# Kernel optimization log

Measured on AMD Instinct MI355X. Metric: run time of the kernel, lower is better.

Reference implementation:

```python
import jax, jax.numpy as jnp
import numpy as np

N_NODES = 50000
N_FEAT = 128
HID = 128
OUT = 64


def setup_inputs() -> dict:
    key = jax.random.key(0)
    ks = jax.random.split(key, 16)
    T, N, F, H, O, E = 8, N_NODES, N_FEAT, HID, OUT, 600000
    s = lambda fan: 1.0 / np.sqrt(fan)
    inp = {
        "x_sequence": jax.random.normal(ks[0], (T, N, F), dtype=jnp.float32),
        "edge_index_sequence": jax.random.randint(ks[1], (T, 2, E), 0, N, dtype=jnp.int64),
        # GCN layer 1 and 2 (weight + bias, PyG GCNConv style)
        "W1": jax.random.uniform(ks[2], (F, H), jnp.float32, -s(F), s(F)),
        "b1": jnp.zeros((H,), jnp.float32),
        "W2": jax.random.uniform(ks[3], (H, H), jnp.float32, -s(H), s(H)),
        "b2": jnp.zeros((H,), jnp.float32),
        # LSTM (single layer, gate order i,f,g,o like torch)
        "Wih": jax.random.uniform(ks[4], (4 * H, H), jnp.float32, -s(H), s(H)),
        "Whh": jax.random.uniform(ks[5], (4 * H, H), jnp.float32, -s(H), s(H)),
        "bih": jax.random.uniform(ks[6], (4 * H,), jnp.float32, -s(H), s(H)),
        "bhh": jax.random.uniform(ks[7], (4 * H,), jnp.float32, -s(H), s(H)),
        # output head
        "Wout": jax.random.uniform(ks[8], (H, O), jnp.float32, -s(H), s(H)),
        "bout": jnp.zeros((O,), jnp.float32),
    }
    return inp


def _gcn(x, src, dst, W, b, n_nodes):
    # GCNConv: add self-loops, symmetric normalization D^-1/2 A D^-1/2
    self_idx = jnp.arange(n_nodes)
    s = jnp.concatenate([src, self_idx])
    d = jnp.concatenate([dst, self_idx])
    deg = jax.ops.segment_sum(jnp.ones(s.shape, x.dtype), d, num_segments=n_nodes)
    dinv = jnp.where(deg > 0, jax.lax.rsqrt(deg), 0.0)
    xw = x @ W                                  # [N,H] transform before aggregation
    coef = (dinv[s] * dinv[d])[:, None]         # [E+N,1]
    agg = jax.ops.segment_sum(xw[s] * coef, d, num_segments=n_nodes)
    return agg + b


def reference(x_sequence, edge_index_sequence, W1, b1, W2, b2,
              Wih, Whh, bih, bhh, Wout, bout):
    T, N, F = x_sequence.shape
    H = Whh.shape[1]

    # spatial GCN stack per timestep (dropout is identity at inference)
    def spatial(carry, inp):
        x_t, ei = inp
        src, dst = ei[0], ei[1]
        h = jax.nn.relu(_gcn(x_t, src, dst, W1, b1, N))
        h = jax.nn.relu(_gcn(h, src, dst, W2, b2, N))
        return carry, h

    _, emb = jax.lax.scan(spatial, None, (x_sequence, edge_index_sequence))  # [T,N,H]

    # LSTM over time, batch = N nodes
    def lstm_step(carry, x_t):
        h, c = carry
        g = x_t @ Wih.T + h @ Whh.T + bih + bhh
        i, f, gg, o = jnp.split(g, 4, axis=-1)
        c = jax.nn.sigmoid(f) * c + jax.nn.sigmoid(i) * jnp.tanh(gg)
        h = jax.nn.sigmoid(o) * jnp.tanh(c)
        return (h, c), None

    h0 = jnp.zeros((N, H), x_sequence.dtype)
    c0 = jnp.zeros((N, H), x_sequence.dtype)
    (hT, cT), _ = jax.lax.scan(lstm_step, (h0, c0), emb)

    final = hT                      # lstm_out[:, -1, :] == last hidden state
    output = final @ Wout + bout    # [N, output_dim]
    return output, hT, cT
```

## Files before the change

kernel.cpp:

```cpp
#include <hip/hip_runtime.h>
#include <math.h>

#define TSTEPS 8
#define FDIM 128
#define HDIM 128
#define ODIM 64
#define GDIM 512
#define BUCKR 2048
#define BUCKR_SHIFT 11
#define BPT 32

typedef __attribute__((ext_vector_type(4))) float f32x4;
typedef __attribute__((ext_vector_type(8))) short s8;

__device__ __forceinline__ float sigmf(float x) { return 1.0f / (1.0f + __expf(-x)); }
__device__ __forceinline__ float fast_tanh(float x) {
    float ax = fabsf(x);
    float ez = __expf(2.f * ax);
    float r = 1.f - 2.f / (ez + 1.f);
    return copysignf(r, x);
}

__device__ __forceinline__ ushort f2bf(float x) {
    uint u = __float_as_uint(x);
    u += 0x7FFFu + ((u >> 16) & 1u);
    return (ushort)(u >> 16);
}
__device__ __forceinline__ float bf2f(ushort h) { return __uint_as_float(((uint)h) << 16); }


__global__ void prep_lstm_w(const float* __restrict__ wih, const float* __restrict__ whh,
                            const float* __restrict__ bih, const float* __restrict__ bhh,
                            float* __restrict__ wcat, float* __restrict__ bsum) {
    int idx = blockIdx.x * 256 + threadIdx.x;
    if (idx < 256 * GDIM) {
        int k = idx >> 9;
        int col = idx & 511;
        float v = (k < HDIM) ? wih[col * HDIM + k] : whh[col * HDIM + (k - HDIM)];
        wcat[idx] = v;
        if (k == 0) bsum[col] = bih[col] + bhh[col];
    }
}

__global__ void pack_b(const float* __restrict__ B, int K, int NC,
                       uint* __restrict__ hi, uint* __restrict__ lo) {
    int total = (K / 32) * (NC / 16) * 256;
    int idx = blockIdx.x * 256 + threadIdx.x;
    if (idx >= total) return;
    int d = idx & 3, l = (idx >> 2) & 63, t = idx >> 8;
    int NT = NC / 16;
    int kt = t / NT, nt = t % NT;
    int k = kt * 32 + (l >> 4) * 8 + d * 2;
    int col = nt * 16 + (l & 15);
    float va = B[(size_t)k * NC + col];
    float vb = B[(size_t)(k + 1) * NC + col];
    ushort ha = f2bf(va), hb = f2bf(vb);
    float ra = va - bf2f(ha), rb = vb - bf2f(hb);
    hi[idx] = (uint)ha | ((uint)hb << 16);
    lo[idx] = (uint)f2bf(ra) | ((uint)f2bf(rb) << 16);
}

__global__ void zero_int(int* __restrict__ p, int n) {
    int idx = blockIdx.x * 256 + threadIdx.x;
    if (idx < n) p[idx] = 0;
}


__global__ __launch_bounds__(256) void bin_count(const int* __restrict__ edges,
                                                 int* __restrict__ gcount,
                                                 int E, int N, int nbuck) {
    __shared__ int h[1024];
    int tid = threadIdx.x;
    int t = blockIdx.x >> 5, b = blockIdx.x & 31;
    int ce = (E + BPT - 1) / BPT;
    int e0 = b * ce, e1 = min(e0 + ce, E);
    for (int i = tid; i < 1024; i += 256) h[i] = 0;
    __syncthreads();
    const int* dstp = edges + (size_t)t * 2 * E + E;
    for (int i = e0 + tid; i < e1; i += 256) {
        int gid = t * N + dstp[i];
        atomicAdd(&h[gid >> BUCKR_SHIFT], 1);
    }
    __syncthreads();
    for (int i = tid; i < nbuck; i += 256) {
        int c = h[i];
        if (c) atomicAdd(&gcount[i], c);
    }
}

__global__ __launch_bounds__(1024) void scan_buckets(const int* __restrict__ gcount,
                                                     int* __restrict__ bucket_start,
                                                     int* __restrict__ bucket_cursor,
                                                     int nbuck, int* __restrict__ row_start,
                                                     int nTotal, int totalE) {
    __shared__ int s[1024];
    int t = threadIdx.x;
    int own = (t < nbuck) ? gcount[t] : 0;
    s[t] = own; __syncthreads();
    for (int off = 1; off < 1024; off <<= 1) {
        int add = (t >= off) ? s[t - off] : 0;
        __syncthreads();
        s[t] += add;
        __syncthreads();
    }
    if (t < nbuck) {
        int excl = s[t] - own;
        bucket_start[t] = excl;
        bucket_cursor[t] = excl;
    }
    if (t == 0) {
        bucket_start[nbuck] = totalE;
        row_start[nTotal] = totalE;
    }
}

__global__ __launch_bounds__(256) void bin_scatter(const int* __restrict__ edges,
                                                   int* __restrict__ bucket_cursor,
                                                   uint2* __restrict__ staged,
                                                   int E, int N, int nbuck) {
    __shared__ int h[1024];
    __shared__ int base[1024];
    int tid = threadIdx.x;
    int t = blockIdx.x >> 5, b = blockIdx.x & 31;
    int ce = (E + BPT - 1) / BPT;
    int e0 = b * ce, e1 = min(e0 + ce, E);
    for (int i = tid; i < 1024; i += 256) h[i] = 0;
    __syncthreads();
    const int* srcp = edges + (size_t)t * 2 * E;
    const int* dstp = srcp + E;
    for (int i = e0 + tid; i < e1; i += 256) {
        int gid = t * N + dstp[i];
        atomicAdd(&h[gid >> BUCKR_SHIFT], 1);
    }
    __syncthreads();
    for (int i = tid; i < nbuck; i += 256) {
        int c = h[i];
        if (c) base[i] = atomicAdd(&bucket_cursor[i], c);
        h[i] = 0;
    }
    __syncthreads();
    for (int i = e0 + tid; i < e1; i += 256) {
        int sgid = t * N + srcp[i];
        int dgid = t * N + dstp[i];
        int bk = dgid >> BUCKR_SHIFT;
        int loc = atomicAdd(&h[bk], 1);
        staged[base[bk] + loc] = make_uint2((uint)sgid, (uint)dgid);
    }
}

__global__ __launch_bounds__(256) void bin_csr(const uint2* __restrict__ staged,
                                               const int* __restrict__ bucket_start,
                                               int* __restrict__ row_start,
                                               int* __restrict__ csr_src,
                                               float* __restrict__ dinv, int nTotal) {
    __shared__ int cnt[BUCKR];
    __shared__ int part[256];
    int tid = threadIdx.x;
    int node0 = blockIdx.x << BUCKR_SHIFT;
    int nloc = min(BUCKR, nTotal - node0);
    int ebase = bucket_start[blockIdx.x], eend = bucket_start[blockIdx.x + 1];

    for (int j = tid; j < BUCKR; j += 256) cnt[j] = 0;
    __syncthreads();
    for (int e = ebase + tid; e < eend; e += 256)
        atomicAdd(&cnt[(int)staged[e].y - node0], 1);
    __syncthreads();

    int s = 0;
    #pragma unroll
    for (int k = 0; k < 8; k++) s += cnt[tid * 8 + k];
    part[tid] = s; __syncthreads();
    for (int off = 1; off < 256; off <<= 1) {
        int add = (tid >= off) ? part[tid - off] : 0;
        __syncthreads();
        part[tid] += add;
        __syncthreads();
    }
    int run = part[tid] - s;
    #pragma unroll
    for (int k = 0; k < 8; k++) {
        int j = tid * 8 + k;
        int c = cnt[j];
        if (j < nloc) {
            row_start[node0 + j] = ebase + run;
            dinv[node0 + j] = rsqrtf((float)(c + 1));
        }
        cnt[j] = run;
        run += c;
    }
    __syncthreads();
    for (int e = ebase + tid; e < eend; e += 256) {
        uint2 ed = staged[e];
        int d = (int)ed.y - node0;
        int pos = ebase + atomicAdd(&cnt[d], 1);
        csr_src[pos] = (int)ed.x;
    }
}


__global__ __launch_bounds__(256) void agg_gather_t(
    const int* __restrict__ row_start, const int* __restrict__ csr_src,
    const uint* __restrict__ xh, const uint* __restrict__ xl,
    const float* __restrict__ dinv, const float* __restrict__ bias,
    uint* __restrict__ ohi, uint* __restrict__ olo, int rowOff, int nloc)
{
    int w = (blockIdx.x * 256 + threadIdx.x) >> 6;
    int lane = threadIdx.x & 63;
    if (w >= nloc) return;
    int wg = rowOff + w;
    float dr = dinv[wg];
    float cc = dr * dr;
    uint shv = xh[(size_t)wg * 64 + lane];
    uint slv = xl[(size_t)wg * 64 + lane];
    float a0 = (__uint_as_float(shv << 16) + __uint_as_float(slv << 16)) * cc;
    float a1 = (__uint_as_float(shv & 0xFFFF0000u) + __uint_as_float(slv & 0xFFFF0000u)) * cc;
    int e = row_start[wg], e1 = row_start[wg + 1];
    for (; e + 4 <= e1; e += 4) {
        int s0 = csr_src[e], s1 = csr_src[e + 1], s2 = csr_src[e + 2], s3 = csr_src[e + 3];
        float c0 = dinv[s0] * dr, c1 = dinv[s1] * dr, c2 = dinv[s2] * dr, c3 = dinv[s3] * dr;
        uint u0 = xh[(size_t)s0 * 64 + lane];
        uint u1 = xh[(size_t)s1 * 64 + lane];
        uint u2 = xh[(size_t)s2 * 64 + lane];
        uint u3 = xh[(size_t)s3 * 64 + lane];
        a0 = fmaf(__uint_as_float(u0 << 16), c0, a0);
        a1 = fmaf(__uint_as_float(u0 & 0xFFFF0000u), c0, a1);
        a0 = fmaf(__uint_as_float(u1 << 16), c1, a0);
        a1 = fmaf(__uint_as_float(u1 & 0xFFFF0000u), c1, a1);
        a0 = fmaf(__uint_as_float(u2 << 16), c2, a0);
        a1 = fmaf(__uint_as_float(u2 & 0xFFFF0000u), c2, a1);
        a0 = fmaf(__uint_as_float(u3 << 16), c3, a0);
        a1 = fmaf(__uint_as_float(u3 & 0xFFFF0000u), c3, a1);
    }
    for (; e < e1; e++) {
        int s = csr_src[e];
        float cf = dinv[s] * dr;
        uint u = xh[(size_t)s * 64 + lane];
        a0 = fmaf(__uint_as_float(u << 16), cf, a0);
        a1 = fmaf(__uint_as_float(u & 0xFFFF0000u), cf, a1);
    }
    float2 b = ((const float2*)bias)[lane];
    a0 = fmaxf(a0 + b.x, 0.f);
    a1 = fmaxf(a1 + b.y, 0.f);
    ushort h0 = f2bf(a0), h1 = f2bf(a1);
    ohi[(size_t)wg * 64 + lane] = (uint)h0 | ((uint)h1 << 16);
    olo[(size_t)wg * 64 + lane] = (uint)f2bf(a0 - bf2f(h0)) | ((uint)f2bf(a1 - bf2f(h1)) << 16);
}


template<bool SPLITSRC>
__global__ __launch_bounds__(512) void gemm_mfma128(
    const float* __restrict__ A32, const ushort* __restrict__ Ahi, const ushort* __restrict__ Alo,
    const uint4* __restrict__ Bhi, const uint4* __restrict__ Blo,
    ushort* __restrict__ Chi, ushort* __restrict__ Clo, int nrows)
{
    __shared__ ushort AsH[128][136];
    __shared__ ushort AsL[128][136];
    const int r0 = blockIdx.x * 128;
    const int tid = threadIdx.x;

    if (SPLITSRC) {
        for (int v = tid; v < 128 * 16; v += 512) {
            int row = v >> 4, seg = v & 15;
            uint4 h = make_uint4(0, 0, 0, 0), L = make_uint4(0, 0, 0, 0);
            if (r0 + row < nrows) {
                h = *(const uint4*)(Ahi + (size_t)(r0 + row) * 128 + seg * 8);
                L = *(const uint4*)(Alo + (size_t)(r0 + row) * 128 + seg * 8);
            }
            *(uint4*)&AsH[row][seg * 8] = h;
            *(uint4*)&AsL[row][seg * 8] = L;
        }
    } else {
        for (int v = tid; v < 128 * 16; v += 512) {
            int row = v >> 4, seg = v & 15;
            float4 a = make_float4(0.f, 0.f, 0.f, 0.f), b = a;
            if (r0 + row < nrows) {
                const float4* src = (const float4*)A32 + (size_t)(r0 + row) * 32 + seg * 2;
                a = src[0]; b = src[1];
            }
            float vv[8] = {a.x, a.y, a.z, a.w, b.x, b.y, b.z, b.w};
            uint hh[4], ll[4];
            #pragma unroll
            for (int i = 0; i < 4; i++) {
                float v0 = vv[2 * i], v1 = vv[2 * i + 1];
                ushort h0 = f2bf(v0), h1 = f2bf(v1);
                hh[i] = (uint)h0 | ((uint)h1 << 16);
                ll[i] = (uint)f2bf(v0 - bf2f(h0)) | ((uint)f2bf(v1 - bf2f(h1)) << 16);
            }
            *(uint4*)&AsH[row][seg * 8] = make_uint4(hh[0], hh[1], hh[2], hh[3]);
            *(uint4*)&AsL[row][seg * 8] = make_uint4(ll[0], ll[1], ll[2], ll[3]);
        }
    }
    __syncthreads();

    const int l = tid & 63, w = tid >> 6;
    const int wm = w & 3, wn = w >> 2;
    const int lrow = l & 15, lk = (l >> 4) * 8;

    f32x4 acc[2][4];
    #pragma unroll
    for (int m = 0; m < 2; m++)
        #pragma unroll
        for (int p = 0; p < 4; p++) acc[m][p] = (f32x4){0.f, 0.f, 0.f, 0.f};

    #pragma unroll
    for (int kt = 0; kt < 4; kt++) {
        uint4 BH[4], BL[4];
        #pragma unroll
        for (int p = 0; p < 4; p++) {
            int nt = 4 * wn + p;
            BH[p] = Bhi[(kt * 8 + nt) * 64 + l];
            BL[p] = Blo[(kt * 8 + nt) * 64 + l];
        }
        s8 aH[2], aL[2];
        #pragma unroll
        for (int m = 0; m < 2; m++) {
            int row = (2 * wm + m) * 16 + lrow;
            aH[m] = *(const s8*)&AsH[row][kt * 32 + lk];
            aL[m] = *(const s8*)&AsL[row][kt * 32 + lk];
        }
        #pragma unroll
        for (int p = 0; p < 4; p++) {
            s8 bh = __builtin_bit_cast(s8, BH[p]);
            s8 bl = __builtin_bit_cast(s8, BL[p]);
            #pragma unroll
            for (int m = 0; m < 2; m++) {
                acc[m][p] = __builtin_amdgcn_mfma_f32_16x16x32_bf16(aH[m], bh, acc[m][p], 0, 0, 0);
                acc[m][p] = __builtin_amdgcn_mfma_f32_16x16x32_bf16(aH[m], bl, acc[m][p], 0, 0, 0);
                acc[m][p] = __builtin_amdgcn_mfma_f32_16x16x32_bf16(aL[m], bh, acc[m][p], 0, 0, 0);
            }
        }
    }

    __syncthreads();
    const int lr4 = (l >> 4) * 4;
    #pragma unroll
    for (int m = 0; m < 2; m++) {
        #pragma unroll
        for (int p = 0; p < 4; p++) {
            int col = (4 * wn + p) * 16 + lrow;
            #pragma unroll
            for (int r = 0; r < 4; r++) {
                int row = (2 * wm + m) * 16 + lr4 + r;
                float v = acc[m][p][r];
                ushort h = f2bf(v);
                AsH[row][col] = h;
                AsL[row][col] = f2bf(v - bf2f(h));
            }
        }
    }
    __syncthreads();
    for (int v = tid; v < 128 * 16; v += 512) {
        int row = v >> 4, seg = v & 15;
        if (r0 + row < nrows) {
            *(uint4*)(Chi + (size_t)(r0 + row) * 128 + seg * 8) = *(const uint4*)&AsH[row][seg * 8];
            *(uint4*)(Clo + (size_t)(r0 + row) * 128 + seg * 8) = *(const uint4*)&AsL[row][seg * 8];
        }
    }
}


template<bool LAST>
__global__ __launch_bounds__(512, 4) void lstm_step_t(
    const ushort* __restrict__ Ehi, const ushort* __restrict__ Elo,
    ushort* __restrict__ Hhi, ushort* __restrict__ Hlo,
    const uint4* __restrict__ Bhi, const uint4* __restrict__ Blo,
    const float* __restrict__ bsum, float* __restrict__ cbuf,
    const uint4* __restrict__ Whi, const uint4* __restrict__ Wlo,
    const float* __restrict__ bout,
    float* __restrict__ outp, float* __restrict__ outh, float* __restrict__ outc,
    int nrows)
{
    __shared__ ushort AsH[32][264];
    __shared__ ushort AsL[32][264];
    const int r0 = blockIdx.x * 32;
    const int tid = threadIdx.x;
    const int l = tid & 63, w = tid >> 6;
    const int lrow = l & 15, lk = (l >> 4) * 8, lr4 = (l >> 4) * 4;

    for (int v = tid; v < 32 * 32; v += 512) {
        int row = v >> 5, seg = v & 31;
        uint4 h = make_uint4(0, 0, 0, 0), L = make_uint4(0, 0, 0, 0);
        if (r0 + row < nrows) {
            if (seg < 16) {
                size_t g = (size_t)(r0 + row) * 128 + seg * 8;
                h = *(const uint4*)(Ehi + g);
                L = *(const uint4*)(Elo + g);
            } else {
                size_t g = (size_t)(r0 + row) * 128 + (seg - 16) * 8;
                h = *(const uint4*)(Hhi + g);
                L = *(const uint4*)(Hlo + g);
            }
        }
        *(uint4*)&AsH[row][seg * 8] = h;
        *(uint4*)&AsL[row][seg * 8] = L;
    }
    __syncthreads();

    f32x4 acc[2][4];
    #pragma unroll
    for (int m = 0; m < 2; m++)
        #pragma unroll
        for (int q = 0; q < 4; q++) {
            float b = bsum[q * 128 + 16 * w + lrow];
            acc[m][q] = (f32x4){b, b, b, b};
        }

    #pragma unroll 2
    for (int kt = 0; kt < 8; kt++) {
        uint4 BH[4], BL[4];
        #pragma unroll
        for (int q = 0; q < 4; q++) {
            int nt = 8 * q + w;
            BH[q] = Bhi[((size_t)kt * 32 + nt) * 64 + l];
            BL[q] = Blo[((size_t)kt * 32 + nt) * 64 + l];
        }
        s8 aH[2], aL[2];
        #pragma unroll
        for (int m = 0; m < 2; m++) {
            int row = m * 16 + lrow;
            aH[m] = *(const s8*)&AsH[row][kt * 32 + lk];
            aL[m] = *(const s8*)&AsL[row][kt * 32 + lk];
        }
        #pragma unroll
        for (int q = 0; q < 4; q++) {
            s8 bh = __builtin_bit_cast(s8, BH[q]);
            s8 bl = __builtin_bit_cast(s8, BL[q]);
            #pragma unroll
            for (int m = 0; m < 2; m++) {
                acc[m][q] = __builtin_amdgcn_mfma_f32_16x16x32_bf16(aH[m], bh, acc[m][q], 0, 0, 0);
                acc[m][q] = __builtin_amdgcn_mfma_f32_16x16x32_bf16(aH[m], bl, acc[m][q], 0, 0, 0);
                acc[m][q] = __builtin_amdgcn_mfma_f32_16x16x32_bf16(aL[m], bh, acc[m][q], 0, 0, 0);
            }
        }
    }
    if (LAST) __syncthreads();

    #pragma unroll
    for (int m = 0; m < 2; m++) {
        int hh = 16 * w + lrow;
        #pragma unroll
        for (int r = 0; r < 4; r++) {
            int row = m * 16 + lr4 + r;
            if (r0 + row < nrows) {
                size_t o = (size_t)(r0 + row) * HDIM + hh;
                float gi = acc[m][0][r], gf = acc[m][1][r];
                float gg = acc[m][2][r], go = acc[m][3][r];
                float cn = sigmf(gf) * cbuf[o] + sigmf(gi) * fast_tanh(gg);
                float hn = sigmf(go) * fast_tanh(cn);
                cbuf[o] = cn;
                ushort hb = f2bf(hn);
                ushort lb = f2bf(hn - bf2f(hb));
                Hhi[o] = hb;
                Hlo[o] = lb;
                if (LAST) {
                    outh[o] = hn;
                    outc[o] = cn;
                    AsH[row][128 + hh] = hb;
                    AsL[row][128 + hh] = lb;
                }
            }
        }
    }

    if (LAST) {
        __syncthreads();
        if (w < 4) {
            f32x4 hacc[2];
            {
                float b = bout[w * 16 + lrow];
                hacc[0] = (f32x4){b, b, b, b};
                hacc[1] = hacc[0];
            }
            #pragma unroll
            for (int kt = 0; kt < 4; kt++) {
                uint4 BH = Whi[(kt * 4 + w) * 64 + l];
                uint4 BL = Wlo[(kt * 4 + w) * 64 + l];
                s8 aH[2], aL[2];
                #pragma unroll
                for (int m = 0; m < 2; m++) {
                    int row = m * 16 + lrow;
                    aH[m] = *(const s8*)&AsH[row][128 + kt * 32 + lk];
                    aL[m] = *(const s8*)&AsL[row][128 + kt * 32 + lk];
                }
                s8 bh = __builtin_bit_cast(s8, BH);
                s8 bl = __builtin_bit_cast(s8, BL);
                #pragma unroll
                for (int m = 0; m < 2; m++) {
                    hacc[m] = __builtin_amdgcn_mfma_f32_16x16x32_bf16(aH[m], bh, hacc[m], 0, 0, 0);
                    hacc[m] = __builtin_amdgcn_mfma_f32_16x16x32_bf16(aH[m], bl, hacc[m], 0, 0, 0);
                    hacc[m] = __builtin_amdgcn_mfma_f32_16x16x32_bf16(aL[m], bh, hacc[m], 0, 0, 0);
                }
            }
            #pragma unroll
            for (int m = 0; m < 2; m++) {
                #pragma unroll
                for (int r = 0; r < 4; r++) {
                    int row = r0 + m * 16 + lr4 + r;
                    if (row < nrows)
                        outp[(size_t)row * ODIM + w * 16 + lrow] = hacc[m][r];
                }
            }
        }
    }
}


static inline int cdiv(long long a, long long b) { return (int)((a + b - 1) / b); }

extern "C" void kernel_launch(void* const* d_in, const int* in_sizes, int n_in,
                              void* d_out, int out_size, void* d_ws, size_t ws_size,
                              hipStream_t stream) {
    const float* x_seq = (const float*)d_in[0];
    const int*   edges = (const int*)d_in[1];
    const float* W1    = (const float*)d_in[2];
    const float* b1    = (const float*)d_in[3];
    const float* W2    = (const float*)d_in[4];
    const float* b2    = (const float*)d_in[5];
    const float* Wih   = (const float*)d_in[6];
    const float* Whh   = (const float*)d_in[7];
    const float* bih   = (const float*)d_in[8];
    const float* bhh   = (const float*)d_in[9];
    const float* Wout  = (const float*)d_in[10];
    const float* bout  = (const float*)d_in[11];
    float* out = (float*)d_out;

    const int N = in_sizes[0] / (TSTEPS * FDIM);
    const int E = in_sizes[1] / (2 * TSTEPS);
    const int NT8 = TSTEPS * N;
    const size_t NP = ((size_t)NT8 + 255) & ~(size_t)255;
    const int NBUCK = cdiv(NT8, BUCKR);
    const size_t nf = (size_t)N * FDIM;
    const int E8 = TSTEPS * E;

    float* ws = (float*)d_ws;
    float* dinv = ws;
    float* wcat = dinv + NP;
    float* bsum = wcat + 131072;
    uint* pW1hi = (uint*)(bsum + 512);
    uint* pW1lo = pW1hi + 8192;
    uint* pW2hi = pW1lo + 8192;
    uint* pW2lo = pW2hi + 8192;
    uint* pWchi = pW2lo + 8192;
    uint* pWclo = pWchi + 65536;
    uint* pWohi = pWclo + 65536;
    uint* pWolo = pWohi + 4096;
    float* cbuf = (float*)(pWolo + 4096);
    ushort* hhi = (ushort*)(cbuf + nf);
    ushort* hlo = hhi + nf;
    ushort* xwhi = hlo + nf;
    ushort* xwlo = xwhi + (size_t)NT8 * 128;
    ushort* h1hi = xwlo + (size_t)NT8 * 128;
    ushort* h1lo = h1hi + (size_t)NT8 * 128;
    ushort* ehi  = h1lo + (size_t)NT8 * 128;
    ushort* elo  = ehi  + (size_t)NT8 * 128;
    uint2* staged  = (uint2*)(elo + (size_t)NT8 * 128);
    int* csr_src   = (int*)(staged + E8);
    int* row_start = csr_src + E8;
    int* gcount    = row_start + NP + 2;
    int* bucket_start  = gcount + 1024;
    int* bucket_cursor = bucket_start + 1026;

    prep_lstm_w<<<cdiv(256 * GDIM, 256), 256, 0, stream>>>(Wih, Whh, bih, bhh, wcat, bsum);
    pack_b<<<32, 256, 0, stream>>>(W1, 128, 128, pW1hi, pW1lo);
    pack_b<<<32, 256, 0, stream>>>(W2, 128, 128, pW2hi, pW2lo);
    pack_b<<<256, 256, 0, stream>>>(wcat, 256, GDIM, pWchi, pWclo);
    pack_b<<<16, 256, 0, stream>>>(Wout, 128, ODIM, pWohi, pWolo);

    zero_int<<<cdiv(2 * (long long)nf, 256), 256, 0, stream>>>((int*)cbuf, (int)(2 * nf));

    zero_int<<<4, 256, 0, stream>>>(gcount, 1024);
    bin_count<<<TSTEPS * BPT, 256, 0, stream>>>(edges, gcount, E, N, NBUCK);
    scan_buckets<<<1, 1024, 0, stream>>>(gcount, bucket_start, bucket_cursor, NBUCK,
                                         row_start, NT8, E8);
    bin_scatter<<<TSTEPS * BPT, 256, 0, stream>>>(edges, bucket_cursor, staged, E, N, NBUCK);
    bin_csr<<<NBUCK, 256, 0, stream>>>(staged, bucket_start, row_start, csr_src, dinv, NT8);

    const int gagrid = cdiv((long long)N * 64, 256);

    gemm_mfma128<false><<<cdiv(NT8, 128), 512, 0, stream>>>(
        x_seq, nullptr, nullptr, (const uint4*)pW1hi, (const uint4*)pW1lo, xwhi, xwlo, NT8);
    for (int t = 0; t < TSTEPS; t++)
        agg_gather_t<<<gagrid, 256, 0, stream>>>(
            row_start, csr_src, (const uint*)xwhi, (const uint*)xwlo, dinv, b1,
            (uint*)h1hi, (uint*)h1lo, t * N, N);

    gemm_mfma128<true><<<cdiv(NT8, 128), 512, 0, stream>>>(
        nullptr, h1hi, h1lo, (const uint4*)pW2hi, (const uint4*)pW2lo, xwhi, xwlo, NT8);
    for (int t = 0; t < TSTEPS; t++)
        agg_gather_t<<<gagrid, 256, 0, stream>>>(
            row_start, csr_src, (const uint*)xwhi, (const uint*)xwlo, dinv, b2,
            (uint*)ehi, (uint*)elo, t * N, N);

    float* out_h = out + (size_t)N * ODIM;
    float* out_c = out_h + (size_t)N * HDIM;
    for (int t = 0; t < TSTEPS - 1; t++) {
        lstm_step_t<false><<<cdiv(N, 32), 512, 0, stream>>>(
            ehi + (size_t)t * N * 128, elo + (size_t)t * N * 128,
            hhi, hlo, (const uint4*)pWchi, (const uint4*)pWclo, bsum, cbuf,
            nullptr, nullptr, nullptr, nullptr, nullptr, nullptr, N);
    }
    lstm_step_t<true><<<cdiv(N, 32), 512, 0, stream>>>(
        ehi + (size_t)(TSTEPS - 1) * N * 128, elo + (size_t)(TSTEPS - 1) * N * 128,
        hhi, hlo, (const uint4*)pWchi, (const uint4*)pWclo, bsum, cbuf,
        (const uint4*)pWohi, (const uint4*)pWolo, bout,
        out, out_h, out_c, N);
}
```

Baseline: 1.593 ms.

## Interleave layer-2 aggregation with LSTM steps using a single-timestep embedding buffer

The second GCN aggregation now writes each timestep's embeddings into one N-row buffer, and the LSTM step for that timestep runs right after it, replacing the buffer that held all T timesteps. The buffer is much smaller and is read soon after being written, so it may still be in the MI355X's last-level cache when the LSTM step reads it, which would cut DRAM traffic. The cost is that aggregation and LSTM launches now alternate, so the stream is strictly serialized and the full-sequence embedding buffer is gone.

```diff
diff --git a/kernel.cpp b/kernel.cpp
--- a/kernel.cpp
+++ b/kernel.cpp
@@ -202,7 +202,7 @@
     const int* __restrict__ row_start, const int* __restrict__ csr_src,
     const uint* __restrict__ xh, const uint* __restrict__ xl,
     const float* __restrict__ dinv, const float* __restrict__ bias,
-    uint* __restrict__ ohi, uint* __restrict__ olo, int rowOff, int nloc)
+    uint* __restrict__ ohi, uint* __restrict__ olo, int rowOff, int outRowOff, int nloc)
 {
     int w = (blockIdx.x * 256 + threadIdx.x) >> 6;
     int lane = threadIdx.x & 63;
@@ -242,8 +242,9 @@
     a0 = fmaxf(a0 + b.x, 0.f);
     a1 = fmaxf(a1 + b.y, 0.f);
     ushort h0 = f2bf(a0), h1 = f2bf(a1);
-    ohi[(size_t)wg * 64 + lane] = (uint)h0 | ((uint)h1 << 16);
-    olo[(size_t)wg * 64 + lane] = (uint)f2bf(a0 - bf2f(h0)) | ((uint)f2bf(a1 - bf2f(h1)) << 16);
+    size_t orow = (size_t)(wg - outRowOff) * 64 + lane;
+    ohi[orow] = (uint)h0 | ((uint)h1 << 16);
+    olo[orow] = (uint)f2bf(a0 - bf2f(h0)) | ((uint)f2bf(a1 - bf2f(h1)) << 16);
 }
 
 
@@ -547,13 +548,13 @@
     float* cbuf = (float*)(pWolo + 4096);
     ushort* hhi = (ushort*)(cbuf + nf);
     ushort* hlo = hhi + nf;
-    ushort* xwhi = hlo + nf;
+    ushort* ehi = hlo + nf;
+    ushort* elo = ehi + nf;
+    ushort* xwhi = elo + nf;
     ushort* xwlo = xwhi + (size_t)NT8 * 128;
     ushort* h1hi = xwlo + (size_t)NT8 * 128;
     ushort* h1lo = h1hi + (size_t)NT8 * 128;
-    ushort* ehi  = h1lo + (size_t)NT8 * 128;
-    ushort* elo  = ehi  + (size_t)NT8 * 128;
-    uint2* staged  = (uint2*)(elo + (size_t)NT8 * 128);
+    uint2* staged  = (uint2*)(h1lo + (size_t)NT8 * 128);
     int* csr_src   = (int*)(staged + E8);
     int* row_start = csr_src + E8;
     int* gcount    = row_start + NP + 2;
@@ -582,26 +583,26 @@
     for (int t = 0; t < TSTEPS; t++)
         agg_gather_t<<<gagrid, 256, 0, stream>>>(
             row_start, csr_src, (const uint*)xwhi, (const uint*)xwlo, dinv, b1,
-            (uint*)h1hi, (uint*)h1lo, t * N, N);
+            (uint*)h1hi, (uint*)h1lo, t * N, 0, N);
 
     gemm_mfma128<true><<<cdiv(NT8, 128), 512, 0, stream>>>(
         nullptr, h1hi, h1lo, (const uint4*)pW2hi, (const uint4*)pW2lo, xwhi, xwlo, NT8);
-    for (int t = 0; t < TSTEPS; t++)
+
+    float* out_h = out + (size_t)N * ODIM;
+    float* out_c = out_h + (size_t)N * HDIM;
+    for (int t = 0; t < TSTEPS; t++) {
         agg_gather_t<<<gagrid, 256, 0, stream>>>(
             row_start, csr_src, (const uint*)xwhi, (const uint*)xwlo, dinv, b2,
-            (uint*)ehi, (uint*)elo, t * N, N);
-
-    float* out_h = out + (size_t)N * ODIM;
-    float* out_c = out_h + (size_t)N * HDIM;
-    for (int t = 0; t < TSTEPS - 1; t++) {
-        lstm_step_t<false><<<cdiv(N, 32), 512, 0, stream>>>(
-            ehi + (size_t)t * N * 128, elo + (size_t)t * N * 128,
-            hhi, hlo, (const uint4*)pWchi, (const uint4*)pWclo, bsum, cbuf,
-            nullptr, nullptr, nullptr, nullptr, nullptr, nullptr, N);
-    }
-    lstm_step_t<true><<<cdiv(N, 32), 512, 0, stream>>>(
-        ehi + (size_t)(TSTEPS - 1) * N * 128, elo + (size_t)(TSTEPS - 1) * N * 128,
-        hhi, hlo, (const uint4*)pWchi, (const uint4*)pWclo, bsum, cbuf,
-        (const uint4*)pWohi, (const uint4*)pWolo, bout,
-        out, out_h, out_c, N);
-}
+            (uint*)ehi, (uint*)elo, t * N, t * N, N);
+        if (t < TSTEPS - 1) {
+            lstm_step_t<false><<<cdiv(N, 32), 512, 0, stream>>>(
+                ehi, elo, hhi, hlo, (const uint4*)pWchi, (const uint4*)pWclo, bsum, cbuf,
+                nullptr, nullptr, nullptr, nullptr, nullptr, nullptr, N);
+        } else {
+            lstm_step_t<true><<<cdiv(N, 32), 512, 0, stream>>>(
+                ehi, elo, hhi, hlo, (const uint4*)pWchi, (const uint4*)pWclo, bsum, cbuf,
+                (const uint4*)pWohi, (const uint4*)pWolo, bout,
+                out, out_h, out_c, N);
+        }
+    }
+}
```

Measured after the change: 1.592 ms. Within noise of the previous version (-0.1%).
